# Optimization experiments

Hardware: AMD Instinct MI355X
Metric: run time of the kernel (lower is better)

Reference implementation:

```python
import jax, jax.numpy as jnp
import numpy as np

C = 512
G = 32  # num_norm_groups
EPS = 1e-6


def setup_inputs() -> dict:
    key = jax.random.key(0)
    ks = jax.random.split(key, 10)
    B, H, W = 8, 64, 64
    s = 1.0 / np.sqrt(C)
    return {
        "x": jax.random.normal(ks[0], (B, C, H, W), dtype=jnp.float32),
        "gamma": jnp.ones((C,), jnp.float32),
        "beta": jnp.zeros((C,), jnp.float32),
        "Wq": jax.random.uniform(ks[1], (C, C), jnp.float32, -s, s),
        "bq": jax.random.uniform(ks[2], (C,), jnp.float32, -s, s),
        "Wk": jax.random.uniform(ks[3], (C, C), jnp.float32, -s, s),
        "bk": jax.random.uniform(ks[4], (C,), jnp.float32, -s, s),
        "Wv": jax.random.uniform(ks[5], (C, C), jnp.float32, -s, s),
        "bv": jax.random.uniform(ks[6], (C,), jnp.float32, -s, s),
        "Wo": jax.random.uniform(ks[7], (C, C), jnp.float32, -s, s),
    }


def group_norm(x, gamma, beta):
    # x: [B, C, H, W]; normalize over each group of C//G channels and all spatial dims
    B, Cc, H, W = x.shape
    xg = x.reshape(B, G, Cc // G, H, W)
    mean = jnp.mean(xg, axis=(2, 3, 4), keepdims=True)
    var = jnp.var(xg, axis=(2, 3, 4), keepdims=True)
    xg = (xg - mean) * jax.lax.rsqrt(var + EPS)
    x = xg.reshape(B, Cc, H, W)
    return x * gamma[None, :, None, None] + beta[None, :, None, None]


def reference(x, gamma, beta, Wq, bq, Wk, bk, Wv, bv, Wo):
    B, Cc, H, W = x.shape
    out = group_norm(x, gamma, beta)
    # [B, C, H, W] -> [B, H*W, C]
    out = out.transpose(0, 2, 3, 1).reshape(B, H * W, Cc)
    q = out @ Wq.T + bq
    k = out @ Wk.T + bk
    v = out @ Wv.T + bv
    score = jnp.einsum('bic,bjc->bij', q, k) / jnp.sqrt(jnp.float32(Cc))
    score = jax.nn.softmax(score, axis=-1)
    out = jnp.einsum('bij,bjc->bic', score, v)
    out = out @ Wo.T
    out = out.reshape(B, H, W, Cc).transpose(0, 3, 1, 2)
    return out + x
```

## Files before the change

kernel.cpp:

```cpp
#include <hip/hip_runtime.h>
#include <hip/hip_bf16.h>
#include <cstdint>
#include <cstddef>

typedef __hip_bfloat16 BF;
typedef __attribute__((ext_vector_type(8))) short bhalf8;
typedef __attribute__((ext_vector_type(4))) float floatx4;

#define NB 8
#define NC 512
#define NHW 4096
#define NG 32

__device__ __forceinline__ float b2f(short h) {
    union { unsigned u; float f; } c;
    c.u = ((unsigned)(unsigned short)h) << 16;
    return c.f;
}
__device__ __forceinline__ short f2b(float f) {
    __hip_bfloat16 h = __float2bfloat16(f);
    short s;
    __builtin_memcpy(&s, &h, 2);
    return s;
}

__device__ __forceinline__ void gload16(const BF* g, BF* l) {
    __builtin_amdgcn_global_load_lds(
        (const __attribute__((address_space(1))) void*)g,
        (__attribute__((address_space(3))) void*)l, 16, 0, 0);
}

__device__ __forceinline__ void BARRIER() {
    asm volatile("" ::: "memory");
    __builtin_amdgcn_s_barrier();
    asm volatile("" ::: "memory");
}
#define WAITVM(N) asm volatile("s_waitcnt vmcnt(" #N ")" ::: "memory")
#define WAITLGKM0() asm volatile("s_waitcnt lgkmcnt(0)" ::: "memory")
#define WAITLGKM8() asm volatile("s_waitcnt lgkmcnt(8)" ::: "memory")
#define SB0() __builtin_amdgcn_sched_barrier(0)

#define DSR(dst, base, IMM) \
    asm volatile("ds_read_b128 %0, %1 offset:" #IMM : "=&v"(dst) : "v"(base))

__device__ __forceinline__ void xcd_swizzle(int& bx, int& by) {
    const int gx = gridDim.x;
    const int nwg = gx * gridDim.y;
    if ((nwg & 7) == 0) {
        const int lin = by * gx + bx;
        const int cpx = nwg >> 3;
        const int s = (lin & 7) * cpx + (lin >> 3);
        bx = s % gx;
        by = s / gx;
    }
}

__global__ __launch_bounds__(256) void f2b_convert4(const float* __restrict__ s0,
                                                    const float* __restrict__ s1,
                                                    const float* __restrict__ s2,
                                                    const float* __restrict__ s3,
                                                    BF* __restrict__ dst) {
    const int which = blockIdx.x >> 8;
    const float* src = (which == 0) ? s0 : (which == 1) ? s1 : (which == 2) ? s2 : s3;
    BF* d = dst + (long)which * (NC * NC);
    const int i = ((blockIdx.x & 255) * 256 + threadIdx.x) * 4;
    float4 v = *(const float4*)&src[i];
    d[i]     = __float2bfloat16(v.x);
    d[i + 1] = __float2bfloat16(v.y);
    d[i + 2] = __float2bfloat16(v.z);
    d[i + 3] = __float2bfloat16(v.w);
}

__global__ __launch_bounds__(256) void gn_stats(const float* __restrict__ x,
                                                float* __restrict__ stats) {
    const int bg = blockIdx.x;
    const long base = (long)bg * 65536;
    float s = 0.f, q = 0.f;
    for (int i = threadIdx.x * 4; i < 65536; i += 256 * 4) {
        float4 v4 = *(const float4*)&x[base + i];
        s += v4.x + v4.y + v4.z + v4.w;
        q += v4.x * v4.x + v4.y * v4.y + v4.z * v4.z + v4.w * v4.w;
    }
#pragma unroll
    for (int o = 32; o; o >>= 1) { s += __shfl_down(s, o); q += __shfl_down(q, o); }
    __shared__ float rs[4], rq[4];
    const int w = threadIdx.x >> 6;
    if ((threadIdx.x & 63) == 0) { rs[w] = s; rq[w] = q; }
    __syncthreads();
    if (threadIdx.x == 0) {
        s = rs[0] + rs[1] + rs[2] + rs[3];
        q = rq[0] + rq[1] + rq[2] + rq[3];
        float mean = s * (1.f / 65536.f);
        float var = q * (1.f / 65536.f) - mean * mean;
        stats[2 * bg]     = mean;
        stats[2 * bg + 1] = rsqrtf(fmaxf(var, 0.f) + 1e-6f);
    }
}

__global__ __launch_bounds__(256) void gn_apply(const float* __restrict__ x,
                                                const float* __restrict__ gamma,
                                                const float* __restrict__ beta,
                                                const float* __restrict__ stats,
                                                BF* __restrict__ n) {
    __shared__ float tile[64][65];
    const int b = blockIdx.z, c0 = blockIdx.y * 64, s0 = blockIdx.x * 64;
    const long xbase = ((long)b * NC + c0) * NHW + s0;
#pragma unroll
    for (int i = 0; i < 16; i++) {
        int lin = i * 256 + threadIdx.x;
        int cl = lin >> 6, sl = lin & 63;
        int c = c0 + cl;
        float2 mr = ((const float2*)stats)[b * NG + (c >> 4)];
        float v = x[xbase + (long)cl * NHW + sl];
        v = (v - mr.x) * mr.y * gamma[c] + beta[c];
        tile[cl][sl] = v;
    }
    __syncthreads();
    const long nbase = ((long)b * NHW + s0) * NC + c0;
#pragma unroll
    for (int i = 0; i < 16; i++) {
        int lin = i * 256 + threadIdx.x;
        int sl = lin >> 6, cl = lin & 63;
        n[nbase + (long)sl * NC + cl] = __float2bfloat16(tile[cl][sl]);
    }
}

#define RD_A_LO(b0, b1) { DSR(aR[0][0],b0,0);    DSR(aR[1][0],b0,2048); \
                          DSR(aR[2][0],b0,4096); DSR(aR[3][0],b0,6144); \
                          DSR(aR[0][1],b1,0);    DSR(aR[1][1],b1,2048); \
                          DSR(aR[2][1],b1,4096); DSR(aR[3][1],b1,6144); }
#define RD_A_HI(b0, b1) { DSR(aR[0][0],b0,8192);  DSR(aR[1][0],b0,10240); \
                          DSR(aR[2][0],b0,12288); DSR(aR[3][0],b0,14336); \
                          DSR(aR[0][1],b1,8192);  DSR(aR[1][1],b1,10240); \
                          DSR(aR[2][1],b1,12288); DSR(aR[3][1],b1,14336); }
#define RD_B_LO(b0, b1) { DSR(bR[0][0],b0,0);    DSR(bR[1][0],b0,2048); \
                          DSR(bR[0][1],b1,0);    DSR(bR[1][1],b1,2048); }
#define RD_B_HI(b0, b1) { DSR(bR[2][0],b0,4096); DSR(bR[3][0],b0,6144); \
                          DSR(bR[2][1],b1,4096); DSR(bR[3][1],b1,6144); }
#define QUAD(M0, N0)                                                                     \
    {                                                                                    \
        _Pragma("unroll") for (int ks = 0; ks < 2; ks++)                                 \
            _Pragma("unroll") for (int mf = (M0); mf < (M0) + 4; mf++)                   \
                _Pragma("unroll") for (int nf = (N0); nf < (N0) + 2; nf++)               \
                    acc[mf][nf] = __builtin_amdgcn_mfma_f32_16x16x32_bf16(               \
                        aR[mf & 3][ks], bR[nf][ks], acc[mf][nf], 0, 0, 0);               \
    }

template <bool BIAS, bool TRANS, bool RESID, bool SPLITK>
__global__ __launch_bounds__(512) void gemm256(
    const BF* __restrict__ A, long aStride,
    const BF* __restrict__ Bm, long bStride,
    BF* __restrict__ C, long cStride,
    const float* __restrict__ bias,
    const float* __restrict__ resid, float* __restrict__ outF,
    int M, int N, int K, float scale, long lda, long ldb)
{
    __shared__ __align__(16) char sL[131072];
    const int tid = threadIdx.x;
    const int wave = tid >> 6, lane = tid & 63;
    int bxi = blockIdx.x, byi = blockIdx.y;
    xcd_swizzle(bxi, byi);
    const int bm = byi * 256, bn = bxi * 256;
    const int zz = blockIdx.z;
    const int bz = SPLITK ? (zz >> 1) : zz;
    const int kh = SPLITK ? (zz & 1) : 0;
    const BF* Ab = A + (long)bz * aStride + (long)kh * K + (long)bm * lda;
    const BF* Bb = Bm + (long)bz * bStride + (long)kh * K + (long)bn * ldb;

    const int d0 = tid * 16, d1 = 8192 + tid * 16;
    const int r0 = d0 >> 7, r1 = d1 >> 7;
    const int c0s = ((d0 ^ ((r0 & 7) << 4)) & 127) >> 1;
    const int c1s = ((d1 ^ ((r1 & 7) << 4)) & 127) >> 1;
    const long sA0 = (long)r0 * lda + c0s, sA1 = (long)r1 * lda + c1s;
    const long sB0 = (long)r0 * ldb + c0s, sB1 = (long)r1 * ldb + c1s;
    const int lds0 = wave * 1024;
    const int lds1 = 8192 + wave * 1024;

    const int lr = lane & 15, lk2 = (lane >> 4) * 16;
    const int swz = (lr & 7) << 4;
    const int sb0 = lr * 128 + (lk2 ^ swz);
    const int sb1 = lr * 128 + ((lk2 + 64) ^ swz);
    const int aReg = (wave >> 2) * 16384;
    const int bReg = (2 + ((wave >> 1) & 1)) * 16384 + (wave & 1) * 8192;
    const int aI0 = aReg + sb0, aI1 = aReg + sb1;
    const int bI0 = bReg + sb0, bI1 = bReg + sb1;
    const int aJ0 = aI0 + 65536, aJ1 = aI1 + 65536;
    const int bJ0 = bI0 + 65536, bJ1 = bI1 + 65536;

    auto STAGE = [&](int t, int region, int dbuf) {
        const bool isA = region < 2;
        const long ld = isA ? lda : ldb;
        const BF* g = (isA ? (Ab + (long)region * 128 * ld)
                           : (Bb + (long)(region - 2) * 128 * ld)) + (long)t * 64;
        char* lb = sL + dbuf * 65536 + region * 16384;
        gload16(g + (isA ? sA0 : sB0), (BF*)(lb + lds0));
        gload16(g + (isA ? sA1 : sB1), (BF*)(lb + lds1));
    };

    floatx4 acc[8][4];
#pragma unroll
    for (int i = 0; i < 8; i++)
#pragma unroll
        for (int j = 0; j < 4; j++) acc[i][j] = (floatx4){0.f, 0.f, 0.f, 0.f};

    const int nt = K >> 6, ngrp = nt >> 1;

    STAGE(0, 0, 0); STAGE(0, 1, 0); STAGE(0, 2, 0); STAGE(0, 3, 0);
    WAITVM(4);
    STAGE(1, 2, 1); STAGE(1, 3, 1); STAGE(1, 0, 1);
    WAITVM(6);
    BARRIER();

    bhalf8 aR[4][2], bR[4][2];

    for (int g = 0; g < ngrp; ++g) {
        const bool st = (g < ngrp - 1);
        const int t2 = 2 * g + 2, t3 = 2 * g + 3;

        RD_A_LO(aI0, aI1);
        RD_B_LO(bI0, bI1);
        if (!(wave & 2)) { RD_B_HI(bI0, bI1); }
        STAGE(2 * g + 1, 1, 1);
        WAITLGKM8();
        BARRIER(); WAITLGKM0(); SB0();
        __builtin_amdgcn_s_setprio(1);
        QUAD(0, 0);
        SB0();
        __builtin_amdgcn_s_setprio(0);
        BARRIER();

        if (wave & 2) { RD_B_HI(bI0, bI1); }
        if (st) STAGE(t2, 2, 0);
        BARRIER(); WAITLGKM0(); SB0();
        __builtin_amdgcn_s_setprio(1);
        QUAD(0, 2);
        SB0();
        __builtin_amdgcn_s_setprio(0);
        BARRIER();

        RD_A_HI(aI0, aI1);
        if (st) STAGE(t2, 3, 0);
        BARRIER(); WAITLGKM0(); SB0();
        __builtin_amdgcn_s_setprio(1);
        QUAD(4, 0);
        SB0();
        __builtin_amdgcn_s_setprio(0);
        BARRIER();

        if (st) STAGE(t2, 0, 0);
        BARRIER(); SB0();
        __builtin_amdgcn_s_setprio(1);
        QUAD(4, 2);
        SB0();
        __builtin_amdgcn_s_setprio(0);
        if (st) { WAITVM(6); } else { WAITVM(0); }
        BARRIER();

        RD_A_LO(aJ0, aJ1);
        RD_B_LO(bJ0, bJ1);
        if (!(wave & 2)) { RD_B_HI(bJ0, bJ1); }
        if (st) STAGE(t2, 1, 0);
        WAITLGKM8();
        BARRIER(); WAITLGKM0(); SB0();
        __builtin_amdgcn_s_setprio(1);
        QUAD(0, 0);
        SB0();
        __builtin_amdgcn_s_setprio(0);
        BARRIER();

        if (wave & 2) { RD_B_HI(bJ0, bJ1); }
        if (st) STAGE(t3, 2, 1);
        BARRIER(); WAITLGKM0(); SB0();
        __builtin_amdgcn_s_setprio(1);
        QUAD(0, 2);
        SB0();
        __builtin_amdgcn_s_setprio(0);
        BARRIER();

        RD_A_HI(aJ0, aJ1);
        if (st) STAGE(t3, 3, 1);
        BARRIER(); WAITLGKM0(); SB0();
        __builtin_amdgcn_s_setprio(1);
        QUAD(4, 0);
        SB0();
        __builtin_amdgcn_s_setprio(0);
        BARRIER();

        if (st) STAGE(t3, 0, 1);
        BARRIER(); SB0();
        __builtin_amdgcn_s_setprio(1);
        QUAD(4, 2);
        SB0();
        __builtin_amdgcn_s_setprio(0);
        if (st) { WAITVM(6); }
        BARRIER();
    }

    const int wm = (wave >> 2) * 128, wn = (wave & 3) * 64;
    if (SPLITK) {
        float* Ob = outF + (long)zz * cStride;
#pragma unroll
        for (int nf = 0; nf < 4; nf++) {
            const int col = bn + wn + nf * 16 + lr;
#pragma unroll
            for (int mf = 0; mf < 8; mf++) {
                const int row0 = bm + wm + mf * 16 + (lane >> 4) * 4;
#pragma unroll
                for (int r = 0; r < 4; r++)
                    Ob[(long)(row0 + r) * N + col] = acc[mf][nf][r] * scale;
            }
        }
        return;
    }
    if (RESID) {
        float* Ob = outF + (long)zz * cStride;
        const float* Xb = resid + (long)zz * cStride;
#pragma unroll
        for (int nf = 0; nf < 4; nf++) {
            const int col = bn + wn + nf * 16 + lr;
#pragma unroll
            for (int mf = 0; mf < 8; mf++) {
                const int row0 = bm + wm + mf * 16 + (lane >> 4) * 4;
                const long a = (long)col * M + row0;
                float4 xv = *(const float4*)&Xb[a];
                float4 ov;
                ov.x = acc[mf][nf][0] * scale + xv.x;
                ov.y = acc[mf][nf][1] * scale + xv.y;
                ov.z = acc[mf][nf][2] * scale + xv.z;
                ov.w = acc[mf][nf][3] * scale + xv.w;
                *(float4*)&Ob[a] = ov;
            }
        }
        return;
    }
    BF* Cb = C + (long)zz * cStride;
#pragma unroll
    for (int nf = 0; nf < 4; nf++) {
        const int col = bn + wn + nf * 16 + lr;
        const float bv = BIAS ? bias[col] : 0.0f;
#pragma unroll
        for (int mf = 0; mf < 8; mf++) {
            const int row0 = bm + wm + mf * 16 + (lane >> 4) * 4;
#pragma unroll
            for (int r = 0; r < 4; r++) {
                float v = acc[mf][nf][r] * scale + bv;
                if (TRANS) Cb[(long)col * M + row0 + r] = __float2bfloat16(v);
                else       Cb[(long)(row0 + r) * N + col] = __float2bfloat16(v);
            }
        }
    }
}

__global__ __launch_bounds__(256) void splitk_reduce(const float* __restrict__ P,
                                                     BF* __restrict__ dst,
                                                     long perBatch) {
    const long off = ((long)blockIdx.x * 256 + threadIdx.x) * 4;
    const float* p0 = P + (long)blockIdx.y * 2 * perBatch;
    float4 a = *(const float4*)&p0[off];
    float4 b = *(const float4*)&p0[perBatch + off];
    BF* d = dst + (long)blockIdx.y * perBatch + off;
    short4 o;
    o.x = f2b(a.x + b.x);
    o.y = f2b(a.y + b.y);
    o.z = f2b(a.z + b.z);
    o.w = f2b(a.w + b.w);
    *(short4*)d = o;
}

template <bool BIAS, bool TRANS>
__global__ __launch_bounds__(256, 2) void gemm128(
    const BF* __restrict__ A, long aStride,
    const BF* __restrict__ Bm, long bStride,
    BF* __restrict__ C, long cStride,
    const float* __restrict__ bias,
    int M, int N, int K, float scale)
{
    __shared__ __align__(16) BF sA[128 * 32];
    __shared__ __align__(16) BF sB[128 * 32];
    const int tid = threadIdx.x;
    const int wave = tid >> 6, lane = tid & 63;
    int bxi = blockIdx.x, byi = blockIdx.y;
    xcd_swizzle(bxi, byi);
    const int bm = byi * 128, bn = bxi * 128;
    const BF* Ab = A + (long)blockIdx.z * aStride + (long)bm * K;
    const BF* Bb = Bm + (long)blockIdx.z * bStride + (long)bn * K;

    const int srow = wave * 32 + (lane >> 2);
    const int sk = (lane & 3) * 8;
    const BF* gA0 = Ab + (long)srow * K + sk;
    const BF* gA1 = gA0 + (long)16 * K;
    const BF* gB0 = Bb + (long)srow * K + sk;
    const BF* gB1 = gB0 + (long)16 * K;
    BF* lA0 = &sA[(wave * 32) * 32];
    BF* lA1 = &sA[(wave * 32 + 16) * 32];
    BF* lB0 = &sB[(wave * 32) * 32];
    BF* lB1 = &sB[(wave * 32 + 16) * 32];

    floatx4 acc[4][4];
#pragma unroll
    for (int i = 0; i < 4; i++)
#pragma unroll
        for (int j = 0; j < 4; j++) acc[i][j] = (floatx4){0.f, 0.f, 0.f, 0.f};

    const int wm = (wave >> 1) * 64, wn = (wave & 1) * 64;
    const int lr = lane & 15, lk = (lane >> 4) * 8;

    for (int k0 = 0; k0 < K; k0 += 32) {
        __syncthreads();
        gload16(gA0 + k0, lA0);
        gload16(gA1 + k0, lA1);
        gload16(gB0 + k0, lB0);
        gload16(gB1 + k0, lB1);
        __syncthreads();
        bhalf8 af[4], bfr[4];
#pragma unroll
        for (int i = 0; i < 4; i++)
            af[i] = *(const bhalf8*)&sA[(wm + i * 16 + lr) * 32 + lk];
#pragma unroll
        for (int i = 0; i < 4; i++)
            bfr[i] = *(const bhalf8*)&sB[(wn + i * 16 + lr) * 32 + lk];
#pragma unroll
        for (int mi = 0; mi < 4; mi++)
#pragma unroll
            for (int ni = 0; ni < 4; ni++)
                acc[mi][ni] = __builtin_amdgcn_mfma_f32_16x16x32_bf16(
                    af[mi], bfr[ni], acc[mi][ni], 0, 0, 0);
    }

    BF* Cb = C + (long)blockIdx.z * cStride;
#pragma unroll
    for (int ni = 0; ni < 4; ni++) {
        const int col = bn + wn + ni * 16 + lr;
        const float bv = BIAS ? bias[col] : 0.0f;
#pragma unroll
        for (int mi = 0; mi < 4; mi++) {
            const int row0 = bm + wm + mi * 16 + (lane >> 4) * 4;
#pragma unroll
            for (int r = 0; r < 4; r++) {
                float v = acc[mi][ni][r] * scale + bv;
                if (TRANS) Cb[(long)col * M + row0 + r] = __float2bfloat16(v);
                else       Cb[(long)(row0 + r) * N + col] = __float2bfloat16(v);
            }
        }
    }
}

__global__ __launch_bounds__(256, 2) void gemm64(
    const BF* __restrict__ A, long aStride,
    const BF* __restrict__ Bm, long bStride,
    BF* __restrict__ C, long cStride,
    int N, int K, float scale)
{
    __shared__ __align__(16) BF sA[64 * 32];
    __shared__ __align__(16) BF sB[128 * 32];
    const int tid = threadIdx.x;
    const int wave = tid >> 6, lane = tid & 63;
    int bxi = blockIdx.x, byi = blockIdx.y;
    xcd_swizzle(bxi, byi);
    const int bm = byi * 64, bn = bxi * 128;
    const BF* Ab = A + (long)blockIdx.z * aStride + (long)bm * K;
    const BF* Bb = Bm + (long)blockIdx.z * bStride + (long)bn * K;

    const int rowoff = lane >> 2, sk = (lane & 3) * 8;
    const BF* gA0 = Ab + (long)(wave * 16 + rowoff) * K + sk;
    const BF* gB0 = Bb + (long)(wave * 32 + rowoff) * K + sk;
    const BF* gB1 = gB0 + (long)16 * K;
    BF* lA0 = &sA[(wave * 16) * 32];
    BF* lB0 = &sB[(wave * 32) * 32];
    BF* lB1 = &sB[(wave * 32 + 16) * 32];

    floatx4 acc[2][4];
#pragma unroll
    for (int i = 0; i < 2; i++)
#pragma unroll
        for (int j = 0; j < 4; j++) acc[i][j] = (floatx4){0.f, 0.f, 0.f, 0.f};

    const int wm = (wave >> 1) * 32, wn = (wave & 1) * 64;
    const int lr = lane & 15, lk = (lane >> 4) * 8;

    for (int k0 = 0; k0 < K; k0 += 32) {
        __syncthreads();
        gload16(gA0 + k0, lA0);
        gload16(gB0 + k0, lB0);
        gload16(gB1 + k0, lB1);
        __syncthreads();
        bhalf8 af[2], bfr[4];
#pragma unroll
        for (int i = 0; i < 2; i++)
            af[i] = *(const bhalf8*)&sA[(wm + i * 16 + lr) * 32 + lk];
#pragma unroll
        for (int i = 0; i < 4; i++)
            bfr[i] = *(const bhalf8*)&sB[(wn + i * 16 + lr) * 32 + lk];
#pragma unroll
        for (int mi = 0; mi < 2; mi++)
#pragma unroll
            for (int ni = 0; ni < 4; ni++)
                acc[mi][ni] = __builtin_amdgcn_mfma_f32_16x16x32_bf16(
                    af[mi], bfr[ni], acc[mi][ni], 0, 0, 0);
    }

    BF* Cb = C + (long)blockIdx.z * cStride;
#pragma unroll
    for (int ni = 0; ni < 4; ni++) {
        const int col = bn + wn + ni * 16 + lr;
#pragma unroll
        for (int mi = 0; mi < 2; mi++) {
            const int row0 = bm + wm + mi * 16 + (lane >> 4) * 4;
#pragma unroll
            for (int r = 0; r < 4; r++)
                Cb[(long)(row0 + r) * N + col] = __float2bfloat16(acc[mi][ni][r] * scale);
        }
    }
}

__global__ __launch_bounds__(256) void softmax4096(BF* __restrict__ S) {
    const long base = (long)blockIdx.x * 4096 + threadIdx.x * 16;
    const int tid = threadIdx.x, w = tid >> 6;
    bhalf8 u = *(bhalf8*)&S[base];
    bhalf8 u2 = *(bhalf8*)&S[base + 8];
    float v[16];
    float m = -1e30f;
#pragma unroll
    for (int j = 0; j < 8; j++) { v[j] = b2f(u[j]); v[8 + j] = b2f(u2[j]); }
#pragma unroll
    for (int j = 0; j < 16; j++) m = fmaxf(m, v[j]);
#pragma unroll
    for (int o = 32; o; o >>= 1) m = fmaxf(m, __shfl_xor(m, o));
    __shared__ float rm[4], rs[4];
    if ((tid & 63) == 0) rm[w] = m;
    __syncthreads();
    m = fmaxf(fmaxf(rm[0], rm[1]), fmaxf(rm[2], rm[3]));
    float s = 0.f;
#pragma unroll
    for (int j = 0; j < 16; j++) { v[j] = __expf(v[j] - m); s += v[j]; }
#pragma unroll
    for (int o = 32; o; o >>= 1) s += __shfl_xor(s, o);
    if ((tid & 63) == 0) rs[w] = s;
    __syncthreads();
    s = rs[0] + rs[1] + rs[2] + rs[3];
    const float inv = 1.0f / s;
#pragma unroll
    for (int j = 0; j < 8; j++) { u[j] = f2b(v[j] * inv); u2[j] = f2b(v[8 + j] * inv); }
    *(bhalf8*)&S[base] = u;
    *(bhalf8*)&S[base + 8] = u2;
}

extern "C" void kernel_launch(void* const* d_in, const int* in_sizes, int n_in,
                              void* d_out, int out_size, void* d_ws, size_t ws_size,
                              hipStream_t stream) {
    const float* x     = (const float*)d_in[0];
    const float* gamma = (const float*)d_in[1];
    const float* beta  = (const float*)d_in[2];
    const float* Wq    = (const float*)d_in[3];
    const float* bq    = (const float*)d_in[4];
    const float* Wk    = (const float*)d_in[5];
    const float* bk    = (const float*)d_in[6];
    const float* Wv    = (const float*)d_in[7];
    const float* bv    = (const float*)d_in[8];
    const float* Wo    = (const float*)d_in[9];
    float* out = (float*)d_out;

    const long ACTB = (long)NHW * NC;
    const long SB   = (long)NHW * NHW;
    const long WSZ  = (long)NC * NC;

    char* ws = (char*)d_ws;
    float* stats = (float*)ws;
    BF* wb = (BF*)(ws + 4096);
    BF* q  = wb + 4 * WSZ;
    BF* kk = q + NB * ACTB;
    BF* vT = kk + NB * ACTB;
    BF* R  = vT + NB * ACTB;
    BF* n = R;
    BF* S = R;

    const size_t base_need = 4096ull + (size_t)4 * WSZ * 2 + (size_t)3 * NB * ACTB * 2;
    long sroom = (ws_size > base_need) ? (long)((ws_size - base_need) / (SB * 2)) : 1;
    int chunk = (int)(sroom < 1 ? 1 : (sroom > NB ? NB : sroom));
    while (NB % chunk) chunk--;

    float* Pf = (float*)(R + (long)chunk * SB);
    const size_t splitNeed = base_need + (size_t)chunk * SB * 2
                           + (size_t)chunk * 2 * ACTB * 4;
    const bool doSplit = (chunk >= 2) && (ws_size >= splitNeed);

    f2b_convert4<<<1024, 256, 0, stream>>>(Wq, Wk, Wv, Wo, wb);

    gn_stats<<<NB * NG, 256, 0, stream>>>(x, stats);
    gn_apply<<<dim3(NHW / 64, NC / 64, NB), 256, 0, stream>>>(x, gamma, beta, stats, n);

    gemm256<true, false, false, false><<<dim3(NC / 256, NHW / 256, NB), 512, 0, stream>>>(
        n, ACTB, wb + 0 * WSZ, 0, q, ACTB, bq, nullptr, nullptr, NHW, NC, NC, 1.0f, NC, NC);
    gemm256<true, false, false, false><<<dim3(NC / 256, NHW / 256, NB), 512, 0, stream>>>(
        n, ACTB, wb + 1 * WSZ, 0, kk, ACTB, bk, nullptr, nullptr, NHW, NC, NC, 1.0f, NC, NC);
    gemm256<true, true, false, false><<<dim3(NC / 256, NHW / 256, NB), 512, 0, stream>>>(
        n, ACTB, wb + 2 * WSZ, 0, vT, ACTB, bv, nullptr, nullptr, NHW, NC, NC, 1.0f, NC, NC);

    const float iscl = 0.044194173824159216f;
    for (int b0 = 0; b0 < NB; b0 += chunk) {
        gemm256<false, false, false, false><<<dim3(NHW / 256, NHW / 256, chunk), 512, 0, stream>>>(
            q + b0 * ACTB, ACTB, kk + b0 * ACTB, ACTB, S, SB, nullptr, nullptr, nullptr,
            NHW, NHW, NC, iscl, NC, NC);
        softmax4096<<<NHW * chunk, 256, 0, stream>>>(S);
        if (doSplit) {
            gemm256<false, false, false, true><<<dim3(NC / 256, NHW / 256, chunk * 2), 512, 0, stream>>>(
                S, SB, vT + b0 * ACTB, ACTB, nullptr, ACTB, nullptr, nullptr, Pf,
                NHW, NC, NHW / 2, 1.0f, NHW, NHW);
            splitk_reduce<<<dim3((unsigned)(ACTB / 1024), chunk), 256, 0, stream>>>(
                Pf, q + b0 * ACTB, ACTB);
        } else if (chunk >= 4) {
            gemm256<false, false, false, false><<<dim3(NC / 256, NHW / 256, chunk), 512, 0, stream>>>(
                S, SB, vT + b0 * ACTB, ACTB, q + b0 * ACTB, ACTB, nullptr, nullptr, nullptr,
                NHW, NC, NHW, 1.0f, NHW, NHW);
        } else if (chunk == 2) {
            gemm128<false, false><<<dim3(NC / 128, NHW / 128, chunk), 256, 0, stream>>>(
                S, SB, vT + b0 * ACTB, ACTB, q + b0 * ACTB, ACTB, nullptr, NHW, NC, NHW, 1.0f);
        } else {
            gemm64<<<dim3(NC / 128, NHW / 64, chunk), 256, 0, stream>>>(
                S, SB, vT + b0 * ACTB, ACTB, q + b0 * ACTB, ACTB, NC, NHW, 1.0f);
        }
    }

    gemm256<false, true, true, false><<<dim3(NC / 256, NHW / 256, NB), 512, 0, stream>>>(
        q, ACTB, wb + 3 * WSZ, 0, nullptr, ACTB, nullptr, x, out, NHW, NC, NC, 1.0f, NC, NC);
}
```

Baseline: 784.3 us.

## Fuse QKV projections into one GEMM, split GN stats, drop split-K PV path

```diff
diff --git a/kernel.cpp b/kernel.cpp
--- a/kernel.cpp
+++ b/kernel.cpp
@@ -37,7 +37,6 @@
 }
 #define WAITVM(N) asm volatile("s_waitcnt vmcnt(" #N ")" ::: "memory")
 #define WAITLGKM0() asm volatile("s_waitcnt lgkmcnt(0)" ::: "memory")
-#define WAITLGKM8() asm volatile("s_waitcnt lgkmcnt(8)" ::: "memory")
 #define SB0() __builtin_amdgcn_sched_barrier(0)
 
 #define DSR(dst, base, IMM) \
@@ -54,6 +53,11 @@
         by = s / gx;
     }
 }
+
+struct QKVPtrs {
+    BF* q; BF* k; BF* v;
+    const float* bq; const float* bk; const float* bv;
+};
 
 __global__ __launch_bounds__(256) void f2b_convert4(const float* __restrict__ s0,
                                                     const float* __restrict__ s1,
@@ -71,12 +75,12 @@
     d[i + 3] = __float2bfloat16(v.w);
 }
 
-__global__ __launch_bounds__(256) void gn_stats(const float* __restrict__ x,
-                                                float* __restrict__ stats) {
-    const int bg = blockIdx.x;
-    const long base = (long)bg * 65536;
+__global__ __launch_bounds__(256) void gn_stats_part(const float* __restrict__ x,
+                                                     float2* __restrict__ part) {
+    const int bg = blockIdx.x, qi = blockIdx.y;
+    const long base = (long)bg * 65536 + (long)qi * 16384;
     float s = 0.f, q = 0.f;
-    for (int i = threadIdx.x * 4; i < 65536; i += 256 * 4) {
+    for (int i = threadIdx.x * 4; i < 16384; i += 256 * 4) {
         float4 v4 = *(const float4*)&x[base + i];
         s += v4.x + v4.y + v4.z + v4.w;
         q += v4.x * v4.x + v4.y * v4.y + v4.z * v4.z + v4.w * v4.w;
@@ -90,11 +94,23 @@
     if (threadIdx.x == 0) {
         s = rs[0] + rs[1] + rs[2] + rs[3];
         q = rq[0] + rq[1] + rq[2] + rq[3];
-        float mean = s * (1.f / 65536.f);
-        float var = q * (1.f / 65536.f) - mean * mean;
-        stats[2 * bg]     = mean;
-        stats[2 * bg + 1] = rsqrtf(fmaxf(var, 0.f) + 1e-6f);
-    }
+        part[bg * 4 + qi] = make_float2(s, q);
+    }
+}
+
+__global__ __launch_bounds__(256) void gn_finalize(const float2* __restrict__ part,
+                                                   float* __restrict__ stats) {
+    const int bg = threadIdx.x;
+    float s = 0.f, q = 0.f;
+#pragma unroll
+    for (int j = 0; j < 4; j++) {
+        float2 p = part[bg * 4 + j];
+        s += p.x; q += p.y;
+    }
+    float mean = s * (1.f / 65536.f);
+    float var = q * (1.f / 65536.f) - mean * mean;
+    stats[2 * bg]     = mean;
+    stats[2 * bg + 1] = rsqrtf(fmaxf(var, 0.f) + 1e-6f);
 }
 
 __global__ __launch_bounds__(256) void gn_apply(const float* __restrict__ x,
@@ -146,14 +162,14 @@
                         aR[mf & 3][ks], bR[nf][ks], acc[mf][nf], 0, 0, 0);               \
     }
 
-template <bool BIAS, bool TRANS, bool RESID, bool SPLITK>
+template <bool BIAS, bool TRANS, bool RESID, bool QKV>
 __global__ __launch_bounds__(512) void gemm256(
     const BF* __restrict__ A, long aStride,
     const BF* __restrict__ Bm, long bStride,
     BF* __restrict__ C, long cStride,
     const float* __restrict__ bias,
     const float* __restrict__ resid, float* __restrict__ outF,
-    int M, int N, int K, float scale, long lda, long ldb)
+    int M, int N, int K, float scale, long lda, long ldb, QKVPtrs P)
 {
     __shared__ __align__(16) char sL[131072];
     const int tid = threadIdx.x;
@@ -162,10 +178,8 @@
     xcd_swizzle(bxi, byi);
     const int bm = byi * 256, bn = bxi * 256;
     const int zz = blockIdx.z;
-    const int bz = SPLITK ? (zz >> 1) : zz;
-    const int kh = SPLITK ? (zz & 1) : 0;
-    const BF* Ab = A + (long)bz * aStride + (long)kh * K + (long)bm * lda;
-    const BF* Bb = Bm + (long)bz * bStride + (long)kh * K + (long)bn * ldb;
+    const BF* Ab = A + (long)zz * aStride + (long)bm * lda;
+    const BF* Bb = Bm + (long)zz * bStride + (long)bn * ldb;
 
     const int d0 = tid * 16, d1 = 8192 + tid * 16;
     const int r0 = d0 >> 7, r1 = d1 >> 7;
@@ -221,11 +235,9 @@
         RD_B_LO(bI0, bI1);
         if (!(wave & 2)) { RD_B_HI(bI0, bI1); }
         STAGE(2 * g + 1, 1, 1);
-        WAITLGKM8();
         BARRIER(); WAITLGKM0(); SB0();
         __builtin_amdgcn_s_setprio(1);
         QUAD(0, 0);
-        SB0();
         __builtin_amdgcn_s_setprio(0);
         BARRIER();
 
@@ -234,7 +246,6 @@
         BARRIER(); WAITLGKM0(); SB0();
         __builtin_amdgcn_s_setprio(1);
         QUAD(0, 2);
-        SB0();
         __builtin_amdgcn_s_setprio(0);
         BARRIER();
 
@@ -243,7 +254,6 @@
         BARRIER(); WAITLGKM0(); SB0();
         __builtin_amdgcn_s_setprio(1);
         QUAD(4, 0);
-        SB0();
         __builtin_amdgcn_s_setprio(0);
         BARRIER();
 
@@ -251,7 +261,6 @@
         BARRIER(); SB0();
         __builtin_amdgcn_s_setprio(1);
         QUAD(4, 2);
-        SB0();
         __builtin_amdgcn_s_setprio(0);
         if (st) { WAITVM(6); } else { WAITVM(0); }
         BARRIER();
@@ -260,11 +269,9 @@
         RD_B_LO(bJ0, bJ1);
         if (!(wave & 2)) { RD_B_HI(bJ0, bJ1); }
         if (st) STAGE(t2, 1, 0);
-        WAITLGKM8();
         BARRIER(); WAITLGKM0(); SB0();
         __builtin_amdgcn_s_setprio(1);
         QUAD(0, 0);
-        SB0();
         __builtin_amdgcn_s_setprio(0);
         BARRIER();
 
@@ -273,7 +280,6 @@
         BARRIER(); WAITLGKM0(); SB0();
         __builtin_amdgcn_s_setprio(1);
         QUAD(0, 2);
-        SB0();
         __builtin_amdgcn_s_setprio(0);
         BARRIER();
 
@@ -282,7 +288,6 @@
         BARRIER(); WAITLGKM0(); SB0();
         __builtin_amdgcn_s_setprio(1);
         QUAD(4, 0);
-        SB0();
         __builtin_amdgcn_s_setprio(0);
         BARRIER();
 
@@ -290,24 +295,30 @@
         BARRIER(); SB0();
         __builtin_amdgcn_s_setprio(1);
         QUAD(4, 2);
-        SB0();
         __builtin_amdgcn_s_setprio(0);
         if (st) { WAITVM(6); }
         BARRIER();
     }
 
     const int wm = (wave >> 2) * 128, wn = (wave & 3) * 64;
-    if (SPLITK) {
-        float* Ob = outF + (long)zz * cStride;
+    if (QKV) {
+        const int sec = bn >> 9;
+        const int cb = bn & 511;
+        BF* Cb = (sec == 0 ? P.q : sec == 1 ? P.k : P.v) + (long)zz * cStride;
+        const float* bb = (sec == 0 ? P.bq : sec == 1 ? P.bk : P.bv);
 #pragma unroll
         for (int nf = 0; nf < 4; nf++) {
-            const int col = bn + wn + nf * 16 + lr;
+            const int col = cb + wn + nf * 16 + lr;
+            const float bvv = bb[col];
 #pragma unroll
             for (int mf = 0; mf < 8; mf++) {
                 const int row0 = bm + wm + mf * 16 + (lane >> 4) * 4;
 #pragma unroll
-                for (int r = 0; r < 4; r++)
-                    Ob[(long)(row0 + r) * N + col] = acc[mf][nf][r] * scale;
+                for (int r = 0; r < 4; r++) {
+                    float v = acc[mf][nf][r] * scale + bvv;
+                    if (sec == 2) Cb[(long)col * M + row0 + r] = __float2bfloat16(v);
+                    else          Cb[(long)(row0 + r) * NC + col] = __float2bfloat16(v);
+                }
             }
         }
         return;
@@ -349,22 +360,6 @@
             }
         }
     }
-}
-
-__global__ __launch_bounds__(256) void splitk_reduce(const float* __restrict__ P,
-                                                     BF* __restrict__ dst,
-                                                     long perBatch) {
-    const long off = ((long)blockIdx.x * 256 + threadIdx.x) * 4;
-    const float* p0 = P + (long)blockIdx.y * 2 * perBatch;
-    float4 a = *(const float4*)&p0[off];
-    float4 b = *(const float4*)&p0[perBatch + off];
-    BF* d = dst + (long)blockIdx.y * perBatch + off;
-    short4 o;
-    o.x = f2b(a.x + b.x);
-    o.y = f2b(a.y + b.y);
-    o.z = f2b(a.z + b.z);
-    o.w = f2b(a.w + b.w);
-    *(short4*)d = o;
 }
 
 template <bool BIAS, bool TRANS>
@@ -566,7 +561,8 @@
 
     char* ws = (char*)d_ws;
     float* stats = (float*)ws;
-    BF* wb = (BF*)(ws + 4096);
+    float2* part = (float2*)(ws + 2048);
+    BF* wb = (BF*)(ws + 16384);
     BF* q  = wb + 4 * WSZ;
     BF* kk = q + NB * ACTB;
     BF* vT = kk + NB * ACTB;
@@ -574,53 +570,38 @@
     BF* n = R;
     BF* S = R;
 
-    const size_t base_need = 4096ull + (size_t)4 * WSZ * 2 + (size_t)3 * NB * ACTB * 2;
+    const size_t base_need = 16384ull + (size_t)4 * WSZ * 2 + (size_t)3 * NB * ACTB * 2;
     long sroom = (ws_size > base_need) ? (long)((ws_size - base_need) / (SB * 2)) : 1;
     int chunk = (int)(sroom < 1 ? 1 : (sroom > NB ? NB : sroom));
     while (NB % chunk) chunk--;
 
-    float* Pf = (float*)(R + (long)chunk * SB);
-    const size_t splitNeed = base_need + (size_t)chunk * SB * 2
-                           + (size_t)chunk * 2 * ACTB * 4;
-    const bool doSplit = (chunk >= 2) && (ws_size >= splitNeed);
+    QKVPtrs qkv = { q, kk, vT, bq, bk, bv };
+    QKVPtrs nil = { nullptr, nullptr, nullptr, nullptr, nullptr, nullptr };
 
     f2b_convert4<<<1024, 256, 0, stream>>>(Wq, Wk, Wv, Wo, wb);
 
-    gn_stats<<<NB * NG, 256, 0, stream>>>(x, stats);
+    gn_stats_part<<<dim3(NB * NG, 4), 256, 0, stream>>>(x, part);
+    gn_finalize<<<1, 256, 0, stream>>>(part, stats);
     gn_apply<<<dim3(NHW / 64, NC / 64, NB), 256, 0, stream>>>(x, gamma, beta, stats, n);
 
-    gemm256<true, false, false, false><<<dim3(NC / 256, NHW / 256, NB), 512, 0, stream>>>(
-        n, ACTB, wb + 0 * WSZ, 0, q, ACTB, bq, nullptr, nullptr, NHW, NC, NC, 1.0f, NC, NC);
-    gemm256<true, false, false, false><<<dim3(NC / 256, NHW / 256, NB), 512, 0, stream>>>(
-        n, ACTB, wb + 1 * WSZ, 0, kk, ACTB, bk, nullptr, nullptr, NHW, NC, NC, 1.0f, NC, NC);
-    gemm256<true, true, false, false><<<dim3(NC / 256, NHW / 256, NB), 512, 0, stream>>>(
-        n, ACTB, wb + 2 * WSZ, 0, vT, ACTB, bv, nullptr, nullptr, NHW, NC, NC, 1.0f, NC, NC);
+    gemm256<false, false, false, true><<<dim3(1536 / 256, NHW / 256, NB), 512, 0, stream>>>(
+        n, ACTB, wb, 0, nullptr, ACTB, nullptr, nullptr, nullptr,
+        NHW, 1536, NC, 1.0f, NC, NC, qkv);
 
     const float iscl = 0.044194173824159216f;
     for (int b0 = 0; b0 < NB; b0 += chunk) {
         gemm256<false, false, false, false><<<dim3(NHW / 256, NHW / 256, chunk), 512, 0, stream>>>(
             q + b0 * ACTB, ACTB, kk + b0 * ACTB, ACTB, S, SB, nullptr, nullptr, nullptr,
-            NHW, NHW, NC, iscl, NC, NC);
+            NHW, NHW, NC, iscl, NC, NC, nil);
         softmax4096<<<NHW * chunk, 256, 0, stream>>>(S);
-        if (doSplit) {
-            gemm256<false, false, false, true><<<dim3(NC / 256, NHW / 256, chunk * 2), 512, 0, stream>>>(
-                S, SB, vT + b0 * ACTB, ACTB, nullptr, ACTB, nullptr, nullptr, Pf,
-                NHW, NC, NHW / 2, 1.0f, NHW, NHW);
-            splitk_reduce<<<dim3((unsigned)(ACTB / 1024), chunk), 256, 0, stream>>>(
-                Pf, q + b0 * ACTB, ACTB);
-        } else if (chunk >= 4) {
-            gemm256<false, false, false, false><<<dim3(NC / 256, NHW / 256, chunk), 512, 0, stream>>>(
-                S, SB, vT + b0 * ACTB, ACTB, q + b0 * ACTB, ACTB, nullptr, nullptr, nullptr,
-                NHW, NC, NHW, 1.0f, NHW, NHW);
-        } else if (chunk == 2) {
+        if (chunk >= 2)
             gemm128<false, false><<<dim3(NC / 128, NHW / 128, chunk), 256, 0, stream>>>(
                 S, SB, vT + b0 * ACTB, ACTB, q + b0 * ACTB, ACTB, nullptr, NHW, NC, NHW, 1.0f);
-        } else {
+        else
             gemm64<<<dim3(NC / 128, NHW / 64, chunk), 256, 0, stream>>>(
                 S, SB, vT + b0 * ACTB, ACTB, q + b0 * ACTB, ACTB, NC, NHW, 1.0f);
-        }
     }
 
     gemm256<false, true, true, false><<<dim3(NC / 256, NHW / 256, NB), 512, 0, stream>>>(
-        q, ACTB, wb + 3 * WSZ, 0, nullptr, ACTB, nullptr, x, out, NHW, NC, NC, 1.0f, NC, NC);
-}
+        q, ACTB, wb + 3 * WSZ, 0, nullptr, ACTB, nullptr, x, out, NHW, NC, NC, 1.0f, NC, NC, nil);
+}
```

Measured after the change: 836.6 us. 6.7% more time.
